# Kernel optimization log

Hardware: AMD Instinct MI355X
Metric: run time of the kernel (lower is better)

The kernel has to match this reference:

```python
import jax, jax.numpy as jnp
import numpy as np

S, B, D, H, DFF = 1024, 4, 1024, 16, 4096
HD = D // H
EPS = 1e-5


def setup_inputs() -> dict:
    key = jax.random.key(0)
    ks = jax.random.split(key, 16)

    def w(k, shape):
        return jax.random.normal(k, shape, jnp.float32) * 0.02

    inp = {
        "input": jax.random.normal(ks[0], (S, B, D), jnp.float32),  # [seq, batch, d_model]
        "enc": jax.random.normal(ks[1], (S, B, D), jnp.float32),
    }
    i = 2
    for pfx in ("sa", "ca"):
        for name in ("wq", "wk", "wv", "wo"):
            inp[f"{pfx}_{name}"] = w(ks[i], (D, D)); i += 1
            inp[f"{pfx}_b{name[1]}"] = jnp.zeros((D,), jnp.float32)
    inp["w1"] = w(ks[i], (DFF, D)); i += 1
    inp["b1"] = jnp.zeros((DFF,), jnp.float32)
    inp["w2"] = w(ks[i], (D, DFF)); i += 1
    inp["b2"] = jnp.zeros((D,), jnp.float32)
    for n in (1, 2, 3):
        inp[f"ln{n}_g"] = jnp.ones((D,), jnp.float32)
        inp[f"ln{n}_b"] = jnp.zeros((D,), jnp.float32)
    return inp


def _layernorm(x, g, b):
    m = x.mean(-1, keepdims=True)
    v = x.var(-1, keepdims=True)
    return (x - m) * jax.lax.rsqrt(v + EPS) * g + b


def _mha(query, key, value, wq, bq, wk, bk, wv, bv, wo, bo):
    # query/key/value: [seq, batch, d_model] (seq-first layout)
    def proj(x, w, b):
        y = x @ w.T + b
        s, bsz, _ = y.shape
        return y.reshape(s, bsz, H, HD)  # [s, b, h, hd]

    q = proj(query, wq, bq)
    k = proj(key, wk, bk)
    v = proj(value, wv, bv)
    scores = jnp.einsum("sbhd,tbhd->bhst", q, k) / (HD ** 0.5)  # [b, h, s_q, s_k]
    p = jax.nn.softmax(scores, axis=-1)
    o = jnp.einsum("bhst,tbhd->sbhd", p, v)  # [s_q, b, h, hd]
    o = o.reshape(o.shape[0], o.shape[1], D)  # heads concatenated along features
    return o @ wo.T + bo  # [s_q, b, d_model]


def reference(input, enc,
              sa_wq, sa_bq, sa_wk, sa_bk, sa_wv, sa_bv, sa_wo, sa_bo,
              ca_wq, ca_bq, ca_wk, ca_bk, ca_wv, ca_bv, ca_wo, ca_bo,
              w1, b1, w2, b2,
              ln1_g, ln1_b, ln2_g, ln2_b, ln3_g, ln3_b):
    # self-attention: attn_in_1(input, input, input) -> q=k=v=input
    out1 = _mha(input, input, input, sa_wq, sa_bq, sa_wk, sa_bk, sa_wv, sa_bv, sa_wo, sa_bo)
    out = _layernorm(input + out1, ln1_g, ln1_b)
    # cross-attention: attn_in_2(out, enc, enc) binds key=out, query=enc, value=enc
    out2 = _mha(enc, out, enc, ca_wq, ca_bq, ca_wk, ca_bk, ca_wv, ca_bv, ca_wo, ca_bo)
    out = _layernorm(out + out2, ln2_g, ln2_b)
    # FFN (dropout is identity at p=0 / eval)
    out3 = jax.nn.relu(out @ w1.T + b1) @ w2.T + b2
    return _layernorm(out + out3, ln3_g, ln3_b)
```

## Files before the change

### kernel.cpp

```cpp
#include <hip/hip_runtime.h>
#include <hip/hip_bf16.h>
#include <cstdint>
#include <cstddef>


typedef __bf16 bf16;
typedef __attribute__((ext_vector_type(8))) __bf16 bf16x8;
typedef __attribute__((ext_vector_type(4))) __bf16 bf16x4;
typedef __attribute__((ext_vector_type(4))) float f32x4;

#define SEQ   1024
#define BATCH 4
#define DMOD  1024
#define NHEAD 16
#define HDIM  64
#define NTOK  (SEQ*BATCH)
#define DFF   4096

#define GLD(gp, lp) __builtin_amdgcn_global_load_lds( \
    (__attribute__((address_space(1))) void*)(gp),    \
    (__attribute__((address_space(3))) void*)(lp), 16, 0, 0)

#define PIN() __builtin_amdgcn_sched_barrier(0)

static __device__ __forceinline__ void pipe_sync() {
  asm volatile("s_waitcnt vmcnt(0)" ::: "memory");
  __builtin_amdgcn_s_barrier();
  asm volatile("" ::: "memory");
}

struct CastSeg { const float* src; bf16* dst; int n4; };
struct CastArgs { CastSeg seg[12]; };

__global__ __launch_bounds__(256) void cast_multi(CastArgs a) {
  CastSeg s = a.seg[blockIdx.y];
  int i = blockIdx.x * 256 + threadIdx.x;
  if (i < s.n4) {
    float4 v = ((const float4*)s.src)[i];
    bf16x4 o; o[0] = (bf16)v.x; o[1] = (bf16)v.y; o[2] = (bf16)v.z; o[3] = (bf16)v.w;
    ((bf16x4*)s.dst)[i] = o;
  }
}

__global__ __launch_bounds__(256) void gemm_nt(
    const bf16* __restrict__ A, const bf16* __restrict__ W,
    const float* __restrict__ b0, const float* __restrict__ b1,
    const float* __restrict__ b2, const float* __restrict__ b3,
    bf16* __restrict__ C, int M, int N, int K, int flags, int kc)
{
  __shared__ bf16 As[2][128 * 64];
  __shared__ bf16 Bs[2][128 * 64];
  const int tid  = threadIdx.x;
  const int wave = tid >> 6, lane = tid & 63;
  const int quad = lane >> 4, l16 = lane & 15;

  const int nbx = gridDim.x, nby = gridDim.y, nbz = gridDim.z;
  const int nbyX = nby >> 3;
  const int lin = blockIdx.x + nbx * (blockIdx.y + nby * blockIdx.z);
  const int c = lin & 7;
  int q = lin >> 3;
  const int by = c * nbyX + (q % nbyX); q /= nbyX;
  const int bx = q % nbx; q /= nbx;
  const int bz = q;

  const int m0 = by * 128, n0 = bx * 128;
  const int wm = (wave >> 1) * 64, wn = (wave & 1) * 64;

  f32x4 acc[4][4] = {};

  const int srow8 = lane >> 3;
  const int sg = ((lane & 7) ^ srow8) * 8;
  const int kbeg = bz * kc;
  const bf16* Ap = A + (size_t)(m0 + wave * 32 + srow8) * K + kbeg + sg;
  const bf16* Wp = W + (size_t)(n0 + wave * 32 + srow8) * K + kbeg + sg;
  const size_t rstep8 = (size_t)8 * K;
  const int woff = (wave * 32) * 64;
  const int fsw = l16 & 7;

  auto stage = [&](bf16* AsD, bf16* BsD, int k0) {
#pragma unroll
    for (int j = 0; j < 4; ++j) {
      GLD(Ap + j * rstep8 + k0, AsD + woff + j * 8 * 64);
      GLD(Wp + j * rstep8 + k0, BsD + woff + j * 8 * 64);
    }
  };
  auto compute = [&](const bf16* AsB, const bf16* BsB) {
#pragma unroll
    for (int ks = 0; ks < 2; ++ks) {
      const int g = ((ks * 4 + quad) ^ fsw) * 8;
      bf16x8 wf[4], tf[4];
#pragma unroll
      for (int i = 0; i < 4; ++i)
        wf[i] = *(const bf16x8*)(BsB + (wn + i * 16 + l16) * 64 + g);
#pragma unroll
      for (int i = 0; i < 4; ++i)
        tf[i] = *(const bf16x8*)(AsB + (wm + i * 16 + l16) * 64 + g);
#pragma unroll
      for (int mi = 0; mi < 4; ++mi)
#pragma unroll
        for (int ni = 0; ni < 4; ++ni)
          acc[mi][ni] = __builtin_amdgcn_mfma_f32_16x16x32_bf16(wf[mi], tf[ni], acc[mi][ni], 0, 0, 0);
    }
  };

  stage(As[0], Bs[0], 0);
  pipe_sync();
  int k0 = 0;
  for (; k0 < kc - 128; k0 += 128) {
    stage(As[1], Bs[1], k0 + 64);
    PIN();
    compute(As[0], Bs[0]);
    pipe_sync();
    stage(As[0], Bs[0], k0 + 128);
    PIN();
    compute(As[1], Bs[1]);
    pipe_sync();
  }
  stage(As[1], Bs[1], k0 + 64);
  PIN();
  compute(As[0], Bs[0]);
  pipe_sync();
  compute(As[1], Bs[1]);

  if (nbz > 1) {
    bf16* Cp = C + (size_t)bz * M * N;
#pragma unroll
    for (int ni = 0; ni < 4; ++ni) {
      const size_t rowb = (size_t)(m0 + wm + ni * 16 + l16) * N;
#pragma unroll
      for (int mi = 0; mi < 4; ++mi) {
        const int gf = n0 + wn + mi * 16 + quad * 4;
        bf16x4 o; o[0] = (bf16)acc[mi][ni][0]; o[1] = (bf16)acc[mi][ni][1];
        o[2] = (bf16)acc[mi][ni][2]; o[3] = (bf16)acc[mi][ni][3];
        *(bf16x4*)(Cp + rowb + gf) = o;
      }
    }
    return;
  }

  const float* bp[4] = {b0, b1, b2, b3};
  const bool orelu = flags & 1;
#pragma unroll
  for (int ni = 0; ni < 4; ++ni) {
    const size_t rowb = (size_t)(m0 + wm + ni * 16 + l16) * N;
#pragma unroll
    for (int mi = 0; mi < 4; ++mi) {
      const int gf = n0 + wn + mi * 16 + quad * 4;
      const float4 bi = *(const float4*)(bp[gf >> 10] + (gf & 1023));
      float v0 = acc[mi][ni][0] + bi.x, v1 = acc[mi][ni][1] + bi.y;
      float v2 = acc[mi][ni][2] + bi.z, v3 = acc[mi][ni][3] + bi.w;
      if (orelu) {
        v0 = fmaxf(v0, 0.f); v1 = fmaxf(v1, 0.f);
        v2 = fmaxf(v2, 0.f); v3 = fmaxf(v3, 0.f);
      }
      bf16x4 o; o[0] = (bf16)v0; o[1] = (bf16)v1; o[2] = (bf16)v2; o[3] = (bf16)v3;
      *(bf16x4*)(C + rowb + gf) = o;
    }
  }
}

__global__ __launch_bounds__(256) void gemm_qkv(
    const bf16* __restrict__ x0b, const bf16* __restrict__ encb,
    const bf16* __restrict__ Wqkv, const bf16* __restrict__ Wqv,
    const float* __restrict__ sbq, const float* __restrict__ sbk,
    const float* __restrict__ sbv,
    const float* __restrict__ cbq, const float* __restrict__ cbv,
    bf16* __restrict__ Qs, bf16* __restrict__ Ks, bf16* __restrict__ VTs,
    bf16* __restrict__ Qc, bf16* __restrict__ VTc)
{
  __shared__ bf16 As[2][128 * 64];
  __shared__ bf16 Bs[2][128 * 64];
  const int tid  = threadIdx.x;
  const int wave = tid >> 6, lane = tid & 63;
  const int quad = lane >> 4, l16 = lane & 15;

  int id = blockIdx.x, seg, bx, by;
  const bf16 *A, *W;
  if (id < 768) {
    seg = 0; const int c = id & 7, q = id >> 3;
    by = c * 4 + (q & 3); bx = q >> 2;
    A = x0b; W = Wqkv;
  } else {
    id -= 768;
    seg = 1; const int c = id & 7, q = id >> 3;
    by = c * 4 + (q & 3); bx = q >> 2;
    A = encb; W = Wqv;
  }
  const int K = 1024;
  const int m0 = by * 128, n0 = bx * 128;
  const int wm = (wave >> 1) * 64, wn = (wave & 1) * 64;

  f32x4 acc[4][4] = {};
  const int srow8 = lane >> 3;
  const int sg = ((lane & 7) ^ srow8) * 8;
  const bf16* Ap = A + (size_t)(m0 + wave * 32 + srow8) * K + sg;
  const bf16* Wp = W + (size_t)(n0 + wave * 32 + srow8) * K + sg;
  const size_t rstep8 = (size_t)8 * K;
  const int woff = (wave * 32) * 64;
  const int fsw = l16 & 7;

  auto stage = [&](bf16* AsD, bf16* BsD, int k0) {
#pragma unroll
    for (int j = 0; j < 4; ++j) {
      GLD(Ap + j * rstep8 + k0, AsD + woff + j * 8 * 64);
      GLD(Wp + j * rstep8 + k0, BsD + woff + j * 8 * 64);
    }
  };
  auto compute = [&](const bf16* AsB, const bf16* BsB) {
#pragma unroll
    for (int ks = 0; ks < 2; ++ks) {
      const int g = ((ks * 4 + quad) ^ fsw) * 8;
      bf16x8 wf[4], tf[4];
#pragma unroll
      for (int i = 0; i < 4; ++i)
        wf[i] = *(const bf16x8*)(BsB + (wn + i * 16 + l16) * 64 + g);
#pragma unroll
      for (int i = 0; i < 4; ++i)
        tf[i] = *(const bf16x8*)(AsB + (wm + i * 16 + l16) * 64 + g);
#pragma unroll
      for (int mi = 0; mi < 4; ++mi)
#pragma unroll
        for (int ni = 0; ni < 4; ++ni)
          acc[mi][ni] = __builtin_amdgcn_mfma_f32_16x16x32_bf16(wf[mi], tf[ni], acc[mi][ni], 0, 0, 0);
    }
  };

  stage(As[0], Bs[0], 0);
  pipe_sync();
  int k0 = 0;
  for (; k0 < K - 128; k0 += 128) {
    stage(As[1], Bs[1], k0 + 64);
    PIN();
    compute(As[0], Bs[0]);
    pipe_sync();
    stage(As[0], Bs[0], k0 + 128);
    PIN();
    compute(As[1], Bs[1]);
    pipe_sync();
  }
  stage(As[1], Bs[1], k0 + 64);
  PIN();
  compute(As[0], Bs[0]);
  pipe_sync();
  compute(As[1], Bs[1]);

  const int region = n0 >> 10;
  const bool isV = (seg == 0) ? (region == 2) : (region == 1);
#pragma unroll
  for (int ni = 0; ni < 4; ++ni) {
    const int i = m0 + wm + ni * 16 + l16;
#pragma unroll
    for (int mi = 0; mi < 4; ++mi) {
      const int gf = n0 + wn + mi * 16 + quad * 4;
      const int lf = gf & 1023;
      if (!isV) {
        if (region == 0) {
          const float* bq = (seg == 0) ? sbq : cbq;
          const float4 bi = *(const float4*)(bq + lf);
          bf16* dst = ((seg == 0) ? Qs : Qc) + (size_t)i * 1024 + lf;
          bf16x4 o;
          o[0] = (bf16)((acc[mi][ni][0] + bi.x) * 0.125f);
          o[1] = (bf16)((acc[mi][ni][1] + bi.y) * 0.125f);
          o[2] = (bf16)((acc[mi][ni][2] + bi.z) * 0.125f);
          o[3] = (bf16)((acc[mi][ni][3] + bi.w) * 0.125f);
          *(bf16x4*)dst = o;
        } else {
          const float4 bi = *(const float4*)(sbk + lf);
          bf16x4 o;
          o[0] = (bf16)(acc[mi][ni][0] + bi.x);
          o[1] = (bf16)(acc[mi][ni][1] + bi.y);
          o[2] = (bf16)(acc[mi][ni][2] + bi.z);
          o[3] = (bf16)(acc[mi][ni][3] + bi.w);
          *(bf16x4*)(Ks + (size_t)i * 1024 + lf) = o;
        }
      } else {
        const float* bv = (seg == 0) ? sbv : cbv;
        const float4 bi = *(const float4*)(bv + lf);
        const int h = lf >> 6, hd = lf & 63;
        const int b = i & 3, s = i >> 2;
        bf16* dst = ((seg == 0) ? VTs : VTc)
                    + (((size_t)b * 16 + h) * 64 + hd) * 1024 + s;
        dst[0]    = (bf16)(acc[mi][ni][0] + bi.x);
        dst[1024] = (bf16)(acc[mi][ni][1] + bi.y);
        dst[2048] = (bf16)(acc[mi][ni][2] + bi.z);
        dst[3072] = (bf16)(acc[mi][ni][3] + bi.w);
      }
    }
  }
}

__global__ __launch_bounds__(256) void attn_kernel(
    const bf16* __restrict__ Q, const bf16* __restrict__ K,
    const bf16* __restrict__ VT, bf16* __restrict__ O)
{
  __shared__ bf16 Kt[2][64 * 64];
  __shared__ bf16 Vt[2][64 * 64];

  const int tid = threadIdx.x, w = tid >> 6, lane = tid & 63;
  const int quad = lane >> 4, l16 = lane & 15;
  const int bh = blockIdx.y, b = bh >> 4;
  const int co = (bh & 15) * HDIM;
  const int sq0 = blockIdx.x * 128 + w * 32;

  bf16x8 qf[2][2];
#pragma unroll
  for (int u = 0; u < 2; ++u) {
    const bf16* qp = Q + ((size_t)(sq0 + u * 16 + l16) * BATCH + b) * 1024 + co + quad * 8;
    qf[u][0] = *(const bf16x8*)qp;
    qf[u][1] = *(const bf16x8*)(qp + 32);
  }

  f32x4 oacc[2][4] = {};
  float lsum[2] = {0.f, 0.f};

  const int srow = lane >> 3;
  const int glog = (lane & 7) ^ srow;
  const int sw = l16 & 7;

  auto stage = [&](bf16* KtD, bf16* VtD, int t0) {
#pragma unroll
    for (int j = 0; j < 2; ++j) {
      const int slot = j * 32 + w * 8 + srow;
      const int m = slot & 15, half = (slot >> 4) & 1, chunk = slot >> 5;
      const int t = chunk * 32 + 8 * (m >> 2) + 4 * half + (m & 3);
      GLD(K + ((size_t)(t0 + t) * BATCH + b) * 1024 + co + glog * 8,
          KtD + (j * 32 + w * 8) * 64);
      const int hd = j * 32 + w * 8 + srow;
      GLD(VT + ((size_t)bh * HDIM + hd) * SEQ + t0 + glog * 8,
          VtD + (j * 32 + w * 8) * 64);
    }
  };

  auto compute = [&](const bf16* KtB, const bf16* VtB) {
#pragma unroll
    for (int c = 0; c < 2; ++c) {
      const bf16* k0 = KtB + (c * 32 + l16) * 64;
      const bf16* k1 = KtB + (c * 32 + 16 + l16) * 64;
      const int g0 = (quad ^ sw) * 8;
      const int g1 = ((4 + quad) ^ sw) * 8;
      bf16x8 ka00 = *(const bf16x8*)(k0 + g0);
      bf16x8 ka01 = *(const bf16x8*)(k0 + g1);
      bf16x8 ka10 = *(const bf16x8*)(k1 + g0);
      bf16x8 ka11 = *(const bf16x8*)(k1 + g1);
      bf16x8 vf[4];
#pragma unroll
      for (int nt = 0; nt < 4; ++nt)
        vf[nt] = *(const bf16x8*)(VtB + (nt * 16 + l16) * 64 + (((c * 4 + quad) ^ sw) * 8));
#pragma unroll
      for (int u = 0; u < 2; ++u) {
        f32x4 c0 = {}, c1 = {};
        c0 = __builtin_amdgcn_mfma_f32_16x16x32_bf16(ka00, qf[u][0], c0, 0, 0, 0);
        c0 = __builtin_amdgcn_mfma_f32_16x16x32_bf16(ka01, qf[u][1], c0, 0, 0, 0);
        c1 = __builtin_amdgcn_mfma_f32_16x16x32_bf16(ka10, qf[u][0], c1, 0, 0, 0);
        c1 = __builtin_amdgcn_mfma_f32_16x16x32_bf16(ka11, qf[u][1], c1, 0, 0, 0);
        bf16x8 pf; float ls = 0.f;
#pragma unroll
        for (int r = 0; r < 4; ++r) {
          float p0 = __expf(c0[r]);
          float p1 = __expf(c1[r]);
          ls += p0 + p1;
          pf[r] = (bf16)p0;
          pf[4 + r] = (bf16)p1;
        }
        lsum[u] += ls;
#pragma unroll
        for (int nt = 0; nt < 4; ++nt)
          oacc[u][nt] = __builtin_amdgcn_mfma_f32_16x16x32_bf16(pf, vf[nt], oacc[u][nt], 0, 0, 0);
      }
    }
  };

  stage(Kt[0], Vt[0], 0);
  pipe_sync();
  int t0 = 0;
  for (; t0 < SEQ - 128; t0 += 128) {
    stage(Kt[1], Vt[1], t0 + 64);
    PIN();
    compute(Kt[0], Vt[0]);
    pipe_sync();
    stage(Kt[0], Vt[0], t0 + 128);
    PIN();
    compute(Kt[1], Vt[1]);
    pipe_sync();
  }
  stage(Kt[1], Vt[1], SEQ - 64);
  PIN();
  compute(Kt[0], Vt[0]);
  pipe_sync();
  compute(Kt[1], Vt[1]);

#pragma unroll
  for (int u = 0; u < 2; ++u) {
    float s = lsum[u];
    s += __shfl_xor(s, 16, 64);
    s += __shfl_xor(s, 32, 64);
#pragma unroll
    for (int r = 0; r < 4; ++r) {
      const float inv = 1.0f / __shfl(s, quad * 4 + r, 64);
      const size_t ro = ((size_t)(sq0 + u * 16 + quad * 4 + r) * BATCH + b) * DMOD + co;
#pragma unroll
      for (int nt = 0; nt < 4; ++nt)
        O[ro + nt * 16 + l16] = (bf16)(oacc[u][nt][r] * inv);
    }
  }
}

__global__ __launch_bounds__(256) void add_ln_red(
    const float* __restrict__ Xa,
    const bf16* __restrict__ p0, const bf16* __restrict__ p1,
    const bf16* __restrict__ p2, const bf16* __restrict__ p3, int np,
    const float* __restrict__ bias,
    const float* __restrict__ g, const float* __restrict__ beta,
    float* __restrict__ outf, bf16* __restrict__ outb)
{
  const int row = blockIdx.x, tid = threadIdx.x;
  const size_t base = (size_t)row * DMOD;
  float4 a = ((const float4*)(Xa + base))[tid];
  bf16x4 q0 = ((const bf16x4*)(p0 + base))[tid];
  bf16x4 q1 = ((const bf16x4*)(p1 + base))[tid];
  float x0 = a.x + (float)q0[0] + (float)q1[0];
  float x1 = a.y + (float)q0[1] + (float)q1[1];
  float x2 = a.z + (float)q0[2] + (float)q1[2];
  float x3 = a.w + (float)q0[3] + (float)q1[3];
  if (np > 2) {
    bf16x4 q2 = ((const bf16x4*)(p2 + base))[tid];
    bf16x4 q3 = ((const bf16x4*)(p3 + base))[tid];
    x0 += (float)q2[0] + (float)q3[0]; x1 += (float)q2[1] + (float)q3[1];
    x2 += (float)q2[2] + (float)q3[2]; x3 += (float)q2[3] + (float)q3[3];
  }
  float4 bi = ((const float4*)bias)[tid];
  x0 += bi.x; x1 += bi.y; x2 += bi.z; x3 += bi.w;

  float s  = x0 + x1 + x2 + x3;
  float s2 = x0 * x0 + x1 * x1 + x2 * x2 + x3 * x3;
#pragma unroll
  for (int m = 1; m < 64; m <<= 1) { s += __shfl_xor(s, m, 64); s2 += __shfl_xor(s2, m, 64); }
  __shared__ float red[8];
  if ((tid & 63) == 0) { red[tid >> 6] = s; red[4 + (tid >> 6)] = s2; }
  __syncthreads();
  s  = red[0] + red[1] + red[2] + red[3];
  s2 = red[4] + red[5] + red[6] + red[7];
  const float mean = s * (1.0f / DMOD);
  const float var  = s2 * (1.0f / DMOD) - mean * mean;
  const float rs   = rsqrtf(var + 1e-5f);
  float4 gv = ((const float4*)g)[tid];
  float4 bv = ((const float4*)beta)[tid];
  float y0 = (x0 - mean) * rs * gv.x + bv.x;
  float y1 = (x1 - mean) * rs * gv.y + bv.y;
  float y2 = (x2 - mean) * rs * gv.z + bv.z;
  float y3 = (x3 - mean) * rs * gv.w + bv.w;
  float4 o; o.x = y0; o.y = y1; o.z = y2; o.w = y3;
  ((float4*)(outf + base))[tid] = o;
  if (outb) {
    bf16x4 ob; ob[0] = (bf16)y0; ob[1] = (bf16)y1; ob[2] = (bf16)y2; ob[3] = (bf16)y3;
    ((bf16x4*)(outb + base))[tid] = ob;
  }
}

__global__ __launch_bounds__(256) void reduce_cast(
    const bf16* __restrict__ p0, const bf16* __restrict__ p1,
    const float* __restrict__ bias, bf16* __restrict__ out)
{
  const int row = blockIdx.x, tid = threadIdx.x;
  const size_t base = (size_t)row * DMOD;
  bf16x4 a = ((const bf16x4*)(p0 + base))[tid];
  bf16x4 b = ((const bf16x4*)(p1 + base))[tid];
  float4 bi = ((const float4*)bias)[tid];
  bf16x4 o;
  o[0] = (bf16)((float)a[0] + (float)b[0] + bi.x);
  o[1] = (bf16)((float)a[1] + (float)b[1] + bi.y);
  o[2] = (bf16)((float)a[2] + (float)b[2] + bi.z);
  o[3] = (bf16)((float)a[3] + (float)b[3] + bi.w);
  ((bf16x4*)(out + base))[tid] = o;
}

extern "C" void kernel_launch(void* const* d_in, const int* in_sizes, int n_in,
                              void* d_out, int out_size, void* d_ws, size_t ws_size,
                              hipStream_t stream)
{
  const float* x0    = (const float*)d_in[0];
  const float* enc   = (const float*)d_in[1];
  const float* sa_wq = (const float*)d_in[2];
  const float* sa_bq = (const float*)d_in[3];
  const float* sa_wk = (const float*)d_in[4];
  const float* sa_bk = (const float*)d_in[5];
  const float* sa_wv = (const float*)d_in[6];
  const float* sa_bv = (const float*)d_in[7];
  const float* sa_wo = (const float*)d_in[8];
  const float* sa_bo = (const float*)d_in[9];
  const float* ca_wq = (const float*)d_in[10];
  const float* ca_bq = (const float*)d_in[11];
  const float* ca_wk = (const float*)d_in[12];
  const float* ca_bk = (const float*)d_in[13];
  const float* ca_wv = (const float*)d_in[14];
  const float* ca_bv = (const float*)d_in[15];
  const float* ca_wo = (const float*)d_in[16];
  const float* ca_bo = (const float*)d_in[17];
  const float* w1    = (const float*)d_in[18];
  const float* b1    = (const float*)d_in[19];
  const float* w2    = (const float*)d_in[20];
  const float* b2    = (const float*)d_in[21];
  const float* ln1g  = (const float*)d_in[22];
  const float* ln1b  = (const float*)d_in[23];
  const float* ln2g  = (const float*)d_in[24];
  const float* ln2b  = (const float*)d_in[25];
  const float* ln3g  = (const float*)d_in[26];
  const float* ln3b  = (const float*)d_in[27];

  char* ws = (char*)d_ws;
  size_t off = 0;
  auto take = [&](size_t bytes) -> char* {
    char* p = ws + off; off += (bytes + 255) & ~(size_t)255; return p;
  };
  const size_t WEL = (size_t)DMOD * DMOD;
  const size_t ACT = (size_t)NTOK * DMOD;
  bf16* Wqkv_s = (bf16*)take(3 * WEL * 2);
  bf16* Wo_s   = (bf16*)take(WEL * 2);
  bf16* Wqv_c  = (bf16*)take(2 * WEL * 2);
  bf16* Wk_c   = (bf16*)take(WEL * 2);
  bf16* Wo_c   = (bf16*)take(WEL * 2);
  bf16* W1b    = (bf16*)take(4 * WEL * 2);
  bf16* W2b    = (bf16*)take(4 * WEL * 2);
  bf16* x0b  = (bf16*)take(ACT * 2);
  bf16* encb = (bf16*)take(ACT * 2);
  bf16* Qs   = (bf16*)take(ACT * 2);
  bf16* Ks   = (bf16*)take(ACT * 2);
  bf16* VTs  = (bf16*)take(ACT * 2);
  bf16* Qc   = (bf16*)take(ACT * 2);
  bf16* VTc  = (bf16*)take(ACT * 2);
  bf16* Kc   = (bf16*)take(ACT * 2);
  bf16* ctx  = (bf16*)take(ACT * 2);
  float* out1f = (float*)take(ACT * 4);
  bf16*  out1b = (bf16*)take(ACT * 2);
  bf16*  Hff   = (bf16*)take((size_t)NTOK * DFF * 2);
  bf16* pA = x0b;  bf16* pB = encb;
  bf16* pC = Qs;   bf16* pD = Ks;
  bf16* f0 = Qs;   bf16* f1 = Ks;  bf16* f2 = VTs;  bf16* f3 = Qc;
  (void)ws_size; (void)in_sizes; (void)n_in; (void)out_size;

  CastArgs cargs;
  const int nw  = (int)(WEL / 4);
  const int ntk = (int)(ACT / 4);
  cargs.seg[0]  = {x0,    x0b,            ntk};
  cargs.seg[1]  = {enc,   encb,           ntk};
  cargs.seg[2]  = {sa_wq, Wqkv_s,         nw};
  cargs.seg[3]  = {sa_wk, Wqkv_s + WEL,   nw};
  cargs.seg[4]  = {sa_wv, Wqkv_s + 2*WEL, nw};
  cargs.seg[5]  = {sa_wo, Wo_s,           nw};
  cargs.seg[6]  = {ca_wq, Wqv_c,          nw};
  cargs.seg[7]  = {ca_wv, Wqv_c + WEL,    nw};
  cargs.seg[8]  = {ca_wk, Wk_c,           nw};
  cargs.seg[9]  = {ca_wo, Wo_c,           nw};
  cargs.seg[10] = {w1,    W1b,            nw * 4};
  cargs.seg[11] = {w2,    W2b,            nw * 4};
  cast_multi<<<dim3((ntk + 255) / 256, 12), 256, 0, stream>>>(cargs);

  auto gemm = [&](const bf16* A, const bf16* Wt,
                  const float* bb0, const float* bb1, const float* bb2, const float* bb3,
                  bf16* Cp, int M, int N, int Kd, int flags, int nz) {
    gemm_nt<<<dim3(N / 128, M / 128, nz), 256, 0, stream>>>(
        A, Wt, bb0, bb1, bb2, bb3, Cp, M, N, Kd, flags, Kd / nz);
  };

  gemm_qkv<<<dim3(1280), 256, 0, stream>>>(
      x0b, encb, Wqkv_s, Wqv_c, sa_bq, sa_bk, sa_bv, ca_bq, ca_bv,
      Qs, Ks, VTs, Qc, VTc);
  attn_kernel<<<dim3(SEQ / 128, BATCH * NHEAD), 256, 0, stream>>>(Qs, Ks, VTs, ctx);
  gemm(ctx, Wo_s, nullptr, nullptr, nullptr, nullptr, pA, NTOK, DMOD, DMOD, 0, 2);
  add_ln_red<<<dim3(NTOK), 256, 0, stream>>>(x0, pA, pB, nullptr, nullptr, 2,
                                             sa_bo, ln1g, ln1b, out1f, out1b);
  gemm(out1b, Wk_c, nullptr, nullptr, nullptr, nullptr, pC, NTOK, DMOD, DMOD, 0, 2);
  reduce_cast<<<dim3(NTOK), 256, 0, stream>>>(pC, pD, ca_bk, Kc);
  attn_kernel<<<dim3(SEQ / 128, BATCH * NHEAD), 256, 0, stream>>>(Qc, Kc, VTc, ctx);
  gemm(ctx, Wo_c, nullptr, nullptr, nullptr, nullptr, pA, NTOK, DMOD, DMOD, 0, 2);
  add_ln_red<<<dim3(NTOK), 256, 0, stream>>>(out1f, pA, pB, nullptr, nullptr, 2,
                                             ca_bo, ln2g, ln2b, out1f, out1b);
  gemm(out1b, W1b, b1, b1 + 1024, b1 + 2048, b1 + 3072, Hff, NTOK, DFF, DMOD, 1, 1);
  gemm(Hff, W2b, nullptr, nullptr, nullptr, nullptr, f0, NTOK, DMOD, DFF, 0, 4);
  add_ln_red<<<dim3(NTOK), 256, 0, stream>>>(out1f, f0, f1, f2, f3, 4,
                                             b2, ln3g, ln3b, (float*)d_out, nullptr);
}
```

Baseline: 476.1 us.

## Add 256x256-tile 8-wave GEMM with interleaved staging for FFN matmuls

Adds a new GEMM kernel with 256x256 output tiles, 512 threads and 8 waves, each wave computing 128x64. Global-to-LDS loads for the next k-tile are split into quarter stages interleaved with MFMA groups, separated by barriers, and the MFMA sections are raised in priority. The kernel is used only for the two FFN GEMMs, with the W2 GEMM keeping a split-K of 4. The intent is more data reuse per LDS load and better overlap of memory traffic with compute, at the cost of more barriers, higher register use and fewer blocks in the grid.

```diff
diff --git a/kernel.cpp b/kernel.cpp
--- a/kernel.cpp
+++ b/kernel.cpp
@@ -22,6 +22,13 @@
     (__attribute__((address_space(3))) void*)(lp), 16, 0, 0)
 
 #define PIN() __builtin_amdgcn_sched_barrier(0)
+#define VM0() asm volatile("s_waitcnt vmcnt(0)" ::: "memory")
+
+static __device__ __forceinline__ void bar() {
+  asm volatile("" ::: "memory");
+  __builtin_amdgcn_s_barrier();
+  asm volatile("" ::: "memory");
+}
 
 static __device__ __forceinline__ void pipe_sync() {
   asm volatile("s_waitcnt vmcnt(0)" ::: "memory");
@@ -42,17 +49,18 @@
   }
 }
 
-__global__ __launch_bounds__(256) void gemm_nt(
+__global__ __launch_bounds__(512, 2) void gemm256(
     const bf16* __restrict__ A, const bf16* __restrict__ W,
     const float* __restrict__ b0, const float* __restrict__ b1,
     const float* __restrict__ b2, const float* __restrict__ b3,
     bf16* __restrict__ C, int M, int N, int K, int flags, int kc)
 {
-  __shared__ bf16 As[2][128 * 64];
-  __shared__ bf16 Bs[2][128 * 64];
+  __shared__ bf16 As[2][2][128 * 64];
+  __shared__ bf16 Bs[2][2][128 * 64];
   const int tid  = threadIdx.x;
-  const int wave = tid >> 6, lane = tid & 63;
+  const int wid  = tid >> 6, lane = tid & 63;
   const int quad = lane >> 4, l16 = lane & 15;
+  const int wfr  = wid >> 2, wtc = wid & 3;
 
   const int nbx = gridDim.x, nby = gridDim.y, nbz = gridDim.z;
   const int nbyX = nby >> 3;
@@ -63,73 +71,100 @@
   const int bx = q % nbx; q /= nbx;
   const int bz = q;
 
-  const int m0 = by * 128, n0 = bx * 128;
-  const int wm = (wave >> 1) * 64, wn = (wave & 1) * 64;
-
-  f32x4 acc[4][4] = {};
-
-  const int srow8 = lane >> 3;
-  const int sg = ((lane & 7) ^ srow8) * 8;
+  const int m0 = by * 256, n0 = bx * 256;
   const int kbeg = bz * kc;
-  const bf16* Ap = A + (size_t)(m0 + wave * 32 + srow8) * K + kbeg + sg;
-  const bf16* Wp = W + (size_t)(n0 + wave * 32 + srow8) * K + kbeg + sg;
-  const size_t rstep8 = (size_t)8 * K;
-  const int woff = (wave * 32) * 64;
+
+  f32x4 acc[8][4] = {};
+
+  const int srow = tid >> 3;
+  const int ssw  = ((tid & 7) ^ (srow & 7)) * 8;
+  const int wslab = (wid * 8) * 64;
+  auto stageH = [&](const bf16* P, int grb, int kt, bf16* ldsH) {
+    const bf16* s0 = P + (size_t)(grb + srow) * K + kbeg + kt * 64 + ssw;
+    GLD(s0, ldsH + wslab);
+    GLD(s0 + (size_t)64 * K, ldsH + 4096 + wslab);
+  };
+
   const int fsw = l16 & 7;
-
-  auto stage = [&](bf16* AsD, bf16* BsD, int k0) {
-#pragma unroll
-    for (int j = 0; j < 4; ++j) {
-      GLD(Ap + j * rstep8 + k0, AsD + woff + j * 8 * 64);
-      GLD(Wp + j * rstep8 + k0, BsD + woff + j * 8 * 64);
-    }
-  };
-  auto compute = [&](const bf16* AsB, const bf16* BsB) {
-#pragma unroll
-    for (int ks = 0; ks < 2; ++ks) {
-      const int g = ((ks * 4 + quad) ^ fsw) * 8;
-      bf16x8 wf[4], tf[4];
-#pragma unroll
-      for (int i = 0; i < 4; ++i)
-        wf[i] = *(const bf16x8*)(BsB + (wn + i * 16 + l16) * 64 + g);
-#pragma unroll
-      for (int i = 0; i < 4; ++i)
-        tf[i] = *(const bf16x8*)(AsB + (wm + i * 16 + l16) * 64 + g);
-#pragma unroll
-      for (int mi = 0; mi < 4; ++mi)
-#pragma unroll
-        for (int ni = 0; ni < 4; ++ni)
-          acc[mi][ni] = __builtin_amdgcn_mfma_f32_16x16x32_bf16(wf[mi], tf[ni], acc[mi][ni], 0, 0, 0);
-    }
-  };
-
-  stage(As[0], Bs[0], 0);
-  pipe_sync();
-  int k0 = 0;
-  for (; k0 < kc - 128; k0 += 128) {
-    stage(As[1], Bs[1], k0 + 64);
-    PIN();
-    compute(As[0], Bs[0]);
-    pipe_sync();
-    stage(As[0], Bs[0], k0 + 128);
-    PIN();
-    compute(As[1], Bs[1]);
-    pipe_sync();
-  }
-  stage(As[1], Bs[1], k0 + 64);
+  bf16x8 tf[4], wf[4];
+  auto ldtf = [&](const bf16* Ah, int ks) {
+    const int g = ((ks * 4 + quad) ^ fsw) * 8;
+#pragma unroll
+    for (int j = 0; j < 4; ++j)
+      tf[j] = *(const bf16x8*)(Ah + ((wtc & 1) * 64 + j * 16 + l16) * 64 + g);
+  };
+  auto ldwf = [&](const bf16* Bh, int mh, int ks) {
+    const int g = ((ks * 4 + quad) ^ fsw) * 8;
+#pragma unroll
+    for (int i = 0; i < 4; ++i)
+      wf[i] = *(const bf16x8*)(Bh + (mh * 64 + i * 16 + l16) * 64 + g);
+  };
+  auto mm = [&](int mh) {
+    __builtin_amdgcn_s_setprio(1);
+#pragma unroll
+    for (int mi = 0; mi < 4; ++mi)
+#pragma unroll
+      for (int ni = 0; ni < 4; ++ni)
+        acc[mh * 4 + mi][ni] =
+            __builtin_amdgcn_mfma_f32_16x16x32_bf16(wf[mi], tf[ni], acc[mh * 4 + mi][ni], 0, 0, 0);
+    __builtin_amdgcn_s_setprio(0);
+  };
+
+  const bf16* Atf0 = &As[0][wtc >> 1][0];
+  const bf16* Atf1 = &As[1][wtc >> 1][0];
+  const bf16* Bwf0 = &Bs[0][wfr][0];
+  const bf16* Bwf1 = &Bs[1][wfr][0];
+
+  const int I = kc >> 7;
+
+  stageH(W, n0 + 0,   0, &Bs[0][0][0]);
+  stageH(W, n0 + 128, 0, &Bs[0][1][0]);
+  stageH(A, m0 + 0,   0, &As[0][0][0]);
+  stageH(A, m0 + 128, 0, &As[0][1][0]);
   PIN();
-  compute(As[0], Bs[0]);
-  pipe_sync();
-  compute(As[1], Bs[1]);
+
+  for (int i = 0; i < I; ++i) {
+    const bool more = (i + 1 < I);
+    const int to = 2 * i + 1;
+    const int tn = 2 * i + 2;
+
+    VM0(); bar();
+    ldtf(Atf0, 0); ldwf(Bwf0, 0, 0);
+    stageH(W, n0 + 0, to, &Bs[1][0][0]);
+    PIN(); bar(); mm(0);
+    ldwf(Bwf0, 1, 0);
+    stageH(W, n0 + 128, to, &Bs[1][1][0]);
+    PIN(); bar(); mm(1);
+    ldtf(Atf0, 1); ldwf(Bwf0, 0, 1);
+    stageH(A, m0 + 0, to, &As[1][0][0]);
+    PIN(); bar(); mm(0);
+    ldwf(Bwf0, 1, 1);
+    stageH(A, m0 + 128, to, &As[1][1][0]);
+    PIN(); bar(); mm(1);
+
+    VM0(); bar();
+    ldtf(Atf1, 0); ldwf(Bwf1, 0, 0);
+    if (more) stageH(W, n0 + 0, tn, &Bs[0][0][0]);
+    PIN(); bar(); mm(0);
+    ldwf(Bwf1, 1, 0);
+    if (more) stageH(W, n0 + 128, tn, &Bs[0][1][0]);
+    PIN(); bar(); mm(1);
+    ldtf(Atf1, 1); ldwf(Bwf1, 0, 1);
+    if (more) stageH(A, m0 + 0, tn, &As[0][0][0]);
+    PIN(); bar(); mm(0);
+    ldwf(Bwf1, 1, 1);
+    if (more) stageH(A, m0 + 128, tn, &As[0][1][0]);
+    PIN(); bar(); mm(1);
+  }
 
   if (nbz > 1) {
     bf16* Cp = C + (size_t)bz * M * N;
 #pragma unroll
     for (int ni = 0; ni < 4; ++ni) {
-      const size_t rowb = (size_t)(m0 + wm + ni * 16 + l16) * N;
-#pragma unroll
-      for (int mi = 0; mi < 4; ++mi) {
-        const int gf = n0 + wn + mi * 16 + quad * 4;
+      const size_t rowb = (size_t)(m0 + wtc * 64 + ni * 16 + l16) * N;
+#pragma unroll
+      for (int mi = 0; mi < 8; ++mi) {
+        const int gf = n0 + wfr * 128 + mi * 16 + quad * 4;
         bf16x4 o; o[0] = (bf16)acc[mi][ni][0]; o[1] = (bf16)acc[mi][ni][1];
         o[2] = (bf16)acc[mi][ni][2]; o[3] = (bf16)acc[mi][ni][3];
         *(bf16x4*)(Cp + rowb + gf) = o;
@@ -142,10 +177,10 @@
   const bool orelu = flags & 1;
 #pragma unroll
   for (int ni = 0; ni < 4; ++ni) {
-    const size_t rowb = (size_t)(m0 + wm + ni * 16 + l16) * N;
-#pragma unroll
-    for (int mi = 0; mi < 4; ++mi) {
-      const int gf = n0 + wn + mi * 16 + quad * 4;
+    const size_t rowb = (size_t)(m0 + wtc * 64 + ni * 16 + l16) * N;
+#pragma unroll
+    for (int mi = 0; mi < 8; ++mi) {
+      const int gf = n0 + wfr * 128 + mi * 16 + quad * 4;
       const float4 bi = *(const float4*)(bp[gf >> 10] + (gf & 1023));
       float v0 = acc[mi][ni][0] + bi.x, v1 = acc[mi][ni][1] + bi.y;
       float v2 = acc[mi][ni][2] + bi.z, v3 = acc[mi][ni][3] + bi.w;
@@ -289,6 +324,123 @@
   }
 }
 
+__global__ __launch_bounds__(256) void gemm_nt(
+    const bf16* __restrict__ A, const bf16* __restrict__ W,
+    const float* __restrict__ b0, const float* __restrict__ b1,
+    const float* __restrict__ b2, const float* __restrict__ b3,
+    bf16* __restrict__ C, int M, int N, int K, int flags, int kc)
+{
+  __shared__ bf16 As[2][128 * 64];
+  __shared__ bf16 Bs[2][128 * 64];
+  const int tid  = threadIdx.x;
+  const int wave = tid >> 6, lane = tid & 63;
+  const int quad = lane >> 4, l16 = lane & 15;
+
+  const int nbx = gridDim.x, nby = gridDim.y, nbz = gridDim.z;
+  const int nbyX = nby >> 3;
+  const int lin = blockIdx.x + nbx * (blockIdx.y + nby * blockIdx.z);
+  const int c = lin & 7;
+  int q = lin >> 3;
+  const int by = c * nbyX + (q % nbyX); q /= nbyX;
+  const int bx = q % nbx; q /= nbx;
+  const int bz = q;
+
+  const int m0 = by * 128, n0 = bx * 128;
+  const int wm = (wave >> 1) * 64, wn = (wave & 1) * 64;
+
+  f32x4 acc[4][4] = {};
+
+  const int srow8 = lane >> 3;
+  const int sg = ((lane & 7) ^ srow8) * 8;
+  const int kbeg = bz * kc;
+  const bf16* Ap = A + (size_t)(m0 + wave * 32 + srow8) * K + kbeg + sg;
+  const bf16* Wp = W + (size_t)(n0 + wave * 32 + srow8) * K + kbeg + sg;
+  const size_t rstep8 = (size_t)8 * K;
+  const int woff = (wave * 32) * 64;
+  const int fsw = l16 & 7;
+
+  auto stage = [&](bf16* AsD, bf16* BsD, int k0) {
+#pragma unroll
+    for (int j = 0; j < 4; ++j) {
+      GLD(Ap + j * rstep8 + k0, AsD + woff + j * 8 * 64);
+      GLD(Wp + j * rstep8 + k0, BsD + woff + j * 8 * 64);
+    }
+  };
+  auto compute = [&](const bf16* AsB, const bf16* BsB) {
+#pragma unroll
+    for (int ks = 0; ks < 2; ++ks) {
+      const int g = ((ks * 4 + quad) ^ fsw) * 8;
+      bf16x8 wf[4], tf[4];
+#pragma unroll
+      for (int i = 0; i < 4; ++i)
+        wf[i] = *(const bf16x8*)(BsB + (wn + i * 16 + l16) * 64 + g);
+#pragma unroll
+      for (int i = 0; i < 4; ++i)
+        tf[i] = *(const bf16x8*)(AsB + (wm + i * 16 + l16) * 64 + g);
+#pragma unroll
+      for (int mi = 0; mi < 4; ++mi)
+#pragma unroll
+        for (int ni = 0; ni < 4; ++ni)
+          acc[mi][ni] = __builtin_amdgcn_mfma_f32_16x16x32_bf16(wf[mi], tf[ni], acc[mi][ni], 0, 0, 0);
+    }
+  };
+
+  stage(As[0], Bs[0], 0);
+  pipe_sync();
+  int k0 = 0;
+  for (; k0 < kc - 128; k0 += 128) {
+    stage(As[1], Bs[1], k0 + 64);
+    PIN();
+    compute(As[0], Bs[0]);
+    pipe_sync();
+    stage(As[0], Bs[0], k0 + 128);
+    PIN();
+    compute(As[1], Bs[1]);
+    pipe_sync();
+  }
+  stage(As[1], Bs[1], k0 + 64);
+  PIN();
+  compute(As[0], Bs[0]);
+  pipe_sync();
+  compute(As[1], Bs[1]);
+
+  if (nbz > 1) {
+    bf16* Cp = C + (size_t)bz * M * N;
+#pragma unroll
+    for (int ni = 0; ni < 4; ++ni) {
+      const size_t rowb = (size_t)(m0 + wm + ni * 16 + l16) * N;
+#pragma unroll
+      for (int mi = 0; mi < 4; ++mi) {
+        const int gf = n0 + wn + mi * 16 + quad * 4;
+        bf16x4 o; o[0] = (bf16)acc[mi][ni][0]; o[1] = (bf16)acc[mi][ni][1];
+        o[2] = (bf16)acc[mi][ni][2]; o[3] = (bf16)acc[mi][ni][3];
+        *(bf16x4*)(Cp + rowb + gf) = o;
+      }
+    }
+    return;
+  }
+
+  const float* bp[4] = {b0, b1, b2, b3};
+  const bool orelu = flags & 1;
+#pragma unroll
+  for (int ni = 0; ni < 4; ++ni) {
+    const size_t rowb = (size_t)(m0 + wm + ni * 16 + l16) * N;
+#pragma unroll
+    for (int mi = 0; mi < 4; ++mi) {
+      const int gf = n0 + wn + mi * 16 + quad * 4;
+      const float4 bi = *(const float4*)(bp[gf >> 10] + (gf & 1023));
+      float v0 = acc[mi][ni][0] + bi.x, v1 = acc[mi][ni][1] + bi.y;
+      float v2 = acc[mi][ni][2] + bi.z, v3 = acc[mi][ni][3] + bi.w;
+      if (orelu) {
+        v0 = fmaxf(v0, 0.f); v1 = fmaxf(v1, 0.f);
+        v2 = fmaxf(v2, 0.f); v3 = fmaxf(v3, 0.f);
+      }
+      bf16x4 o; o[0] = (bf16)v0; o[1] = (bf16)v1; o[2] = (bf16)v2; o[3] = (bf16)v3;
+      *(bf16x4*)(C + rowb + gf) = o;
+    }
+  }
+}
+
 __global__ __launch_bounds__(256) void attn_kernel(
     const bf16* __restrict__ Q, const bf16* __restrict__ K,
     const bf16* __restrict__ VT, bf16* __restrict__ O)
@@ -575,8 +727,10 @@
   gemm(ctx, Wo_c, nullptr, nullptr, nullptr, nullptr, pA, NTOK, DMOD, DMOD, 0, 2);
   add_ln_red<<<dim3(NTOK), 256, 0, stream>>>(out1f, pA, pB, nullptr, nullptr, 2,
                                              ca_bo, ln2g, ln2b, out1f, out1b);
-  gemm(out1b, W1b, b1, b1 + 1024, b1 + 2048, b1 + 3072, Hff, NTOK, DFF, DMOD, 1, 1);
-  gemm(Hff, W2b, nullptr, nullptr, nullptr, nullptr, f0, NTOK, DMOD, DFF, 0, 4);
+  gemm256<<<dim3(DFF / 256, NTOK / 256, 1), 512, 0, stream>>>(
+      out1b, W1b, b1, b1 + 1024, b1 + 2048, b1 + 3072, Hff, NTOK, DFF, DMOD, 1, DMOD);
+  gemm256<<<dim3(DMOD / 256, NTOK / 256, 4), 512, 0, stream>>>(
+      Hff, W2b, nullptr, nullptr, nullptr, nullptr, f0, NTOK, DMOD, DFF, 0, DFF / 4);
   add_ln_red<<<dim3(NTOK), 256, 0, stream>>>(out1f, f0, f1, f2, f3, 4,
                                              b2, ln3g, ln3b, (float*)d_out, nullptr);
 }
```

Measured after the change: 485.6 us. No clear change (+2.0%).
